# Optimization experiments

Measured on AMD Instinct MI355X. Metric: run time of the kernel, lower is better.

## Reference

```python
import jax, jax.numpy as jnp
import numpy as np


def setup_inputs() -> dict:
    key = jax.random.key(0)
    k1, k2 = jax.random.split(key)
    B, S, D = 4, 8192, 1024
    x = jax.random.normal(k1, (B, S, D), dtype=jnp.float32)
    alpha = jax.random.uniform(k2, (B, S, D), dtype=jnp.float32)
    return {"x": x, "alpha": alpha}


def reference(x, alpha):
    # Linear recurrence h_t = alpha_t * h_{t-1} + x_t, computed as an
    # associative scan over the sequence axis (axis=1).
    def linear_combine(i, j):
        x_i, a_i = i
        x_j, a_j = j
        return (a_j * x_i + x_j, a_j * a_i)

    ys, _ = jax.lax.associative_scan(linear_combine, (x, alpha), axis=1)
    return ys
```

## Files before the change

kernel.cpp:

```cpp
#include <hip/hip_runtime.h>

constexpr int B  = 4;
constexpr int S  = 8192;
constexpr int D  = 1024;
constexpr int C  = 512;
constexpr int L  = S / C;
constexpr int D4 = D / 4;

typedef float nt_float4 __attribute__((ext_vector_type(4)));

__global__ __launch_bounds__(256, 8) void phase1(const float4* __restrict__ x,
                                                 const float4* __restrict__ a,
                                                 float4* __restrict__ Xagg,
                                                 float4* __restrict__ Aagg) {
    const int t = threadIdx.x;
    const int c = blockIdx.x;
    const int b = blockIdx.y;
    const long base = ((long)(b * S + c * L)) * D4 + t;

    float4 X = {0.f, 0.f, 0.f, 0.f};
    float4 A = {1.f, 1.f, 1.f, 1.f};
    #pragma unroll 4
    for (int s = 0; s < L; ++s) {
        float4 xv = x[base + (long)s * D4];
        float4 av = a[base + (long)s * D4];
        X.x = fmaf(av.x, X.x, xv.x);
        X.y = fmaf(av.y, X.y, xv.y);
        X.z = fmaf(av.z, X.z, xv.z);
        X.w = fmaf(av.w, X.w, xv.w);
        A.x *= av.x; A.y *= av.y; A.z *= av.z; A.w *= av.w;
    }
    const long o = ((long)(b * C + c)) * D4 + t;
    Xagg[o] = X;
    Aagg[o] = A;
}

__global__ __launch_bounds__(64) void phase2(float* __restrict__ Xagg,
                                             const float* __restrict__ Aagg) {
    const int g = blockIdx.x * 64 + threadIdx.x;
    const int b = g >> 10;
    const int d = g & (D - 1);
    float*       Xp = Xagg + (long)b * C * D + d;
    const float* Ap = Aagg + (long)b * C * D + d;
    float carry = 0.f;
    for (int c = 0; c < C; c += 4) {
        const long o0 = (long)c * D, o1 = o0 + D, o2 = o1 + D, o3 = o2 + D;
        const float X0 = Xp[o0], X1 = Xp[o1], X2 = Xp[o2], X3 = Xp[o3];
        const float A0 = Ap[o0], A1 = Ap[o1], A2 = Ap[o2], A3 = Ap[o3];
        Xp[o0] = carry; carry = fmaf(A0, carry, X0);
        Xp[o1] = carry; carry = fmaf(A1, carry, X1);
        Xp[o2] = carry; carry = fmaf(A2, carry, X2);
        Xp[o3] = carry; carry = fmaf(A3, carry, X3);
    }
}

__global__ __launch_bounds__(256, 8) void phase3(const float4* __restrict__ x,
                                                 const float4* __restrict__ a,
                                                 const float4* __restrict__ prefix,
                                                 float4* __restrict__ out) {
    const int t = threadIdx.x;
    const int c = blockIdx.x;
    const int b = blockIdx.y;

    float4 h = prefix[((long)(b * C + c)) * D4 + t];
    const long base = ((long)(b * S + c * L)) * D4 + t;
    nt_float4* ntout = (nt_float4*)out;
    #pragma unroll 4
    for (int s = 0; s < L; ++s) {
        float4 xv = x[base + (long)s * D4];
        float4 av = a[base + (long)s * D4];
        h.x = fmaf(av.x, h.x, xv.x);
        h.y = fmaf(av.y, h.y, xv.y);
        h.z = fmaf(av.z, h.z, xv.z);
        h.w = fmaf(av.w, h.w, xv.w);
        nt_float4 hv = {h.x, h.y, h.z, h.w};
        __builtin_nontemporal_store(hv, &ntout[base + (long)s * D4]);
    }
}

extern "C" void kernel_launch(void* const* d_in, const int* in_sizes, int n_in,
                              void* d_out, int out_size, void* d_ws, size_t ws_size,
                              hipStream_t stream) {
    const float4* x = (const float4*)d_in[0];
    const float4* a = (const float4*)d_in[1];
    float4* out = (float4*)d_out;

    float* Xagg = (float*)d_ws;
    float* Aagg = Xagg + (size_t)B * C * D;

    dim3 grid1(C, B);
    phase1<<<grid1, 256, 0, stream>>>(x, a, (float4*)Xagg, (float4*)Aagg);

    phase2<<<(B * D) / 64, 64, 0, stream>>>(Xagg, Aagg);

    phase3<<<grid1, 256, 0, stream>>>(x, a, (const float4*)Xagg, out);
}
```

Baseline: 374.7 us.

## Fuse three-phase scan into single-pass decoupled look-back kernel

Replaces the three kernels (chunk reduce, carry scan, chunk rescan) with a single kernel. It uses a dynamic ticket for block ordering and decoupled look-back through flags that mark whether a chunk's aggregate or its inclusive carry is ready. Each block keeps its 16 timesteps of x and alpha in registers, so the inputs are read from global memory once instead of twice, and two kernel launches go away. In exchange it adds serial dependency chains across blocks with spin-waiting, higher register pressure that lowers occupancy, and a workspace memset on every call.

```diff
diff --git a/kernel.cpp b/kernel.cpp
--- a/kernel.cpp
+++ b/kernel.cpp
@@ -6,74 +6,113 @@
 constexpr int C  = 512;
 constexpr int L  = S / C;
 constexpr int D4 = D / 4;
+constexpr int R  = B * C;
 
 typedef float nt_float4 __attribute__((ext_vector_type(4)));
 
-__global__ __launch_bounds__(256, 8) void phase1(const float4* __restrict__ x,
-                                                 const float4* __restrict__ a,
-                                                 float4* __restrict__ Xagg,
-                                                 float4* __restrict__ Aagg) {
+__device__ __forceinline__ void store2(unsigned long long* p, float a, float b) {
+    union { float f[2]; unsigned long long u; } v; v.f[0] = a; v.f[1] = b;
+    __hip_atomic_store(p, v.u, __ATOMIC_RELAXED, __HIP_MEMORY_SCOPE_AGENT);
+}
+__device__ __forceinline__ void load2(unsigned long long* p, float& a, float& b) {
+    union { float f[2]; unsigned long long u; } v;
+    v.u = __hip_atomic_load(p, __ATOMIC_RELAXED, __HIP_MEMORY_SCOPE_AGENT);
+    a = v.f[0]; b = v.f[1];
+}
+
+__global__ __launch_bounds__(256, 2) void scan_fused(const float4* __restrict__ x,
+                                                     const float4* __restrict__ a,
+                                                     float4* __restrict__ out,
+                                                     unsigned long long* __restrict__ Xagg,
+                                                     unsigned long long* __restrict__ Aagg,
+                                                     unsigned long long* __restrict__ Carr,
+                                                     int* __restrict__ flags,
+                                                     int* __restrict__ ticket) {
     const int t = threadIdx.x;
-    const int c = blockIdx.x;
-    const int b = blockIdx.y;
+    __shared__ int svid;
+    if (t == 0) svid = atomicAdd(ticket, 1);
+    __syncthreads();
+    const int vid = svid;
+    const int b = vid & (B - 1);
+    const int c = vid >> 2;
+    const int r = b * C + c;
+
     const long base = ((long)(b * S + c * L)) * D4 + t;
 
-    float4 X = {0.f, 0.f, 0.f, 0.f};
-    float4 A = {1.f, 1.f, 1.f, 1.f};
-    #pragma unroll 4
+    float4 Xs[L], Ps[L];
+    #pragma unroll
     for (int s = 0; s < L; ++s) {
-        float4 xv = x[base + (long)s * D4];
-        float4 av = a[base + (long)s * D4];
-        X.x = fmaf(av.x, X.x, xv.x);
-        X.y = fmaf(av.y, X.y, xv.y);
-        X.z = fmaf(av.z, X.z, xv.z);
-        X.w = fmaf(av.w, X.w, xv.w);
-        A.x *= av.x; A.y *= av.y; A.z *= av.z; A.w *= av.w;
+        Xs[s] = x[base + (long)s * D4];
+        Ps[s] = a[base + (long)s * D4];
     }
-    const long o = ((long)(b * C + c)) * D4 + t;
-    Xagg[o] = X;
-    Aagg[o] = A;
-}
+    #pragma unroll
+    for (int s = 1; s < L; ++s) {
+        Xs[s].x = fmaf(Ps[s].x, Xs[s-1].x, Xs[s].x);
+        Xs[s].y = fmaf(Ps[s].y, Xs[s-1].y, Xs[s].y);
+        Xs[s].z = fmaf(Ps[s].z, Xs[s-1].z, Xs[s].z);
+        Xs[s].w = fmaf(Ps[s].w, Xs[s-1].w, Xs[s].w);
+        Ps[s].x *= Ps[s-1].x; Ps[s].y *= Ps[s-1].y;
+        Ps[s].z *= Ps[s-1].z; Ps[s].w *= Ps[s-1].w;
+    }
 
-__global__ __launch_bounds__(64) void phase2(float* __restrict__ Xagg,
-                                             const float* __restrict__ Aagg) {
-    const int g = blockIdx.x * 64 + threadIdx.x;
-    const int b = g >> 10;
-    const int d = g & (D - 1);
-    float*       Xp = Xagg + (long)b * C * D + d;
-    const float* Ap = Aagg + (long)b * C * D + d;
-    float carry = 0.f;
-    for (int c = 0; c < C; c += 4) {
-        const long o0 = (long)c * D, o1 = o0 + D, o2 = o1 + D, o3 = o2 + D;
-        const float X0 = Xp[o0], X1 = Xp[o1], X2 = Xp[o2], X3 = Xp[o3];
-        const float A0 = Ap[o0], A1 = Ap[o1], A2 = Ap[o2], A3 = Ap[o3];
-        Xp[o0] = carry; carry = fmaf(A0, carry, X0);
-        Xp[o1] = carry; carry = fmaf(A1, carry, X1);
-        Xp[o2] = carry; carry = fmaf(A2, carry, X2);
-        Xp[o3] = carry; carry = fmaf(A3, carry, X3);
+    if (c > 0) {
+        const long o = ((long)r * D4 + t) * 2;
+        store2(Xagg + o,     Xs[L-1].x, Xs[L-1].y);
+        store2(Xagg + o + 1, Xs[L-1].z, Xs[L-1].w);
+        store2(Aagg + o,     Ps[L-1].x, Ps[L-1].y);
+        store2(Aagg + o + 1, Ps[L-1].z, Ps[L-1].w);
+        __syncthreads();
+        if (t == 0) __hip_atomic_store(&flags[r], 1, __ATOMIC_RELEASE, __HIP_MEMORY_SCOPE_AGENT);
     }
-}
 
-__global__ __launch_bounds__(256, 8) void phase3(const float4* __restrict__ x,
-                                                 const float4* __restrict__ a,
-                                                 const float4* __restrict__ prefix,
-                                                 float4* __restrict__ out) {
-    const int t = threadIdx.x;
-    const int c = blockIdx.x;
-    const int b = blockIdx.y;
+    float4 carry = {0.f, 0.f, 0.f, 0.f};
+    if (c > 0) {
+        float4 Ar = {1.f, 1.f, 1.f, 1.f};
+        float4 Xr = {0.f, 0.f, 0.f, 0.f};
+        for (int k = r - 1;;) {
+            int f;
+            while ((f = __hip_atomic_load(&flags[k], __ATOMIC_RELAXED,
+                                          __HIP_MEMORY_SCOPE_AGENT)) == 0)
+                __builtin_amdgcn_s_sleep(1);
+            const long o = ((long)k * D4 + t) * 2;
+            if (f == 2) {
+                float cx, cy, cz, cw;
+                load2(Carr + o, cx, cy); load2(Carr + o + 1, cz, cw);
+                carry.x = fmaf(Ar.x, cx, Xr.x);
+                carry.y = fmaf(Ar.y, cy, Xr.y);
+                carry.z = fmaf(Ar.z, cz, Xr.z);
+                carry.w = fmaf(Ar.w, cw, Xr.w);
+                break;
+            }
+            float4 Xk, Ak;
+            load2(Xagg + o, Xk.x, Xk.y); load2(Xagg + o + 1, Xk.z, Xk.w);
+            load2(Aagg + o, Ak.x, Ak.y); load2(Aagg + o + 1, Ak.z, Ak.w);
+            Xr.x = fmaf(Ar.x, Xk.x, Xr.x); Xr.y = fmaf(Ar.y, Xk.y, Xr.y);
+            Xr.z = fmaf(Ar.z, Xk.z, Xr.z); Xr.w = fmaf(Ar.w, Xk.w, Xr.w);
+            Ar.x *= Ak.x; Ar.y *= Ak.y; Ar.z *= Ak.z; Ar.w *= Ak.w;
+            --k;
+        }
+    }
 
-    float4 h = prefix[((long)(b * C + c)) * D4 + t];
-    const long base = ((long)(b * S + c * L)) * D4 + t;
+    {
+        const long o = ((long)r * D4 + t) * 2;
+        float4 co;
+        co.x = fmaf(Ps[L-1].x, carry.x, Xs[L-1].x);
+        co.y = fmaf(Ps[L-1].y, carry.y, Xs[L-1].y);
+        co.z = fmaf(Ps[L-1].z, carry.z, Xs[L-1].z);
+        co.w = fmaf(Ps[L-1].w, carry.w, Xs[L-1].w);
+        store2(Carr + o, co.x, co.y); store2(Carr + o + 1, co.z, co.w);
+    }
+    __syncthreads();
+    if (t == 0) __hip_atomic_store(&flags[r], 2, __ATOMIC_RELEASE, __HIP_MEMORY_SCOPE_AGENT);
+
     nt_float4* ntout = (nt_float4*)out;
-    #pragma unroll 4
+    #pragma unroll
     for (int s = 0; s < L; ++s) {
-        float4 xv = x[base + (long)s * D4];
-        float4 av = a[base + (long)s * D4];
-        h.x = fmaf(av.x, h.x, xv.x);
-        h.y = fmaf(av.y, h.y, xv.y);
-        h.z = fmaf(av.z, h.z, xv.z);
-        h.w = fmaf(av.w, h.w, xv.w);
-        nt_float4 hv = {h.x, h.y, h.z, h.w};
+        nt_float4 hv = { fmaf(Ps[s].x, carry.x, Xs[s].x),
+                         fmaf(Ps[s].y, carry.y, Xs[s].y),
+                         fmaf(Ps[s].z, carry.z, Xs[s].z),
+                         fmaf(Ps[s].w, carry.w, Xs[s].w) };
         __builtin_nontemporal_store(hv, &ntout[base + (long)s * D4]);
     }
 }
@@ -85,13 +124,13 @@
     const float4* a = (const float4*)d_in[1];
     float4* out = (float4*)d_out;
 
-    float* Xagg = (float*)d_ws;
-    float* Aagg = Xagg + (size_t)B * C * D;
+    char* ws = (char*)d_ws;
+    int* ticket = (int*)ws;
+    int* flags  = (int*)(ws + 256);
+    unsigned long long* Xagg = (unsigned long long*)(ws + 16384);
+    unsigned long long* Aagg = Xagg + (size_t)R * D4 * 2;
+    unsigned long long* Carr = Aagg + (size_t)R * D4 * 2;
 
-    dim3 grid1(C, B);
-    phase1<<<grid1, 256, 0, stream>>>(x, a, (float4*)Xagg, (float4*)Aagg);
-
-    phase2<<<(B * D) / 64, 64, 0, stream>>>(Xagg, Aagg);
-
-    phase3<<<grid1, 256, 0, stream>>>(x, a, (const float4*)Xagg, out);
+    hipMemsetAsync(ws, 0, 16384, stream);
+    scan_fused<<<dim3(R), 256, 0, stream>>>(x, a, out, Xagg, Aagg, Carr, flags, ticket);
 }
```

New measurement: 550.1 us. +46.8%, slower.

## Fuse three scan phases into one persistent kernel with grid barriers

Applied to the files above, without the earlier changes.

Replaces the three-kernel chunked scan with a single kernel of 256 blocks that syncs through atomic grid barriers. Chunks become longer (128 steps), which shrinks the carry scan across chunks. Loads are issued in double-buffered groups of 8 to keep more memory requests in flight. The change removes launch gaps and the intermediate round trip, but it depends on all 256 blocks being resident at once and adds a memset plus spin barriers. Only 256 blocks of one wave each run, so occupancy drops and memory parallelism may suffer.

```diff
diff --git a/kernel.cpp b/kernel.cpp
--- a/kernel.cpp
+++ b/kernel.cpp
@@ -1,80 +1,145 @@
 #include <hip/hip_runtime.h>
 
-constexpr int B  = 4;
-constexpr int S  = 8192;
-constexpr int D  = 1024;
-constexpr int C  = 512;
-constexpr int L  = S / C;
-constexpr int D4 = D / 4;
+constexpr int B    = 4;
+constexpr int S    = 8192;
+constexpr int D    = 1024;
+constexpr int CB   = 64;
+constexpr int L    = S / CB;
+constexpr int D4   = D / 4;
+constexpr int NBLK = B * CB;
+constexpr int G    = 8;
+constexpr int NG   = L / G;
 
 typedef float nt_float4 __attribute__((ext_vector_type(4)));
 
-__global__ __launch_bounds__(256, 8) void phase1(const float4* __restrict__ x,
-                                                 const float4* __restrict__ a,
-                                                 float4* __restrict__ Xagg,
-                                                 float4* __restrict__ Aagg) {
-    const int t = threadIdx.x;
-    const int c = blockIdx.x;
-    const int b = blockIdx.y;
+__device__ __forceinline__ void ast(float* p, float v) {
+    __hip_atomic_store(p, v, __ATOMIC_RELAXED, __HIP_MEMORY_SCOPE_AGENT);
+}
+__device__ __forceinline__ float ald(const float* p) {
+    return __hip_atomic_load(p, __ATOMIC_RELAXED, __HIP_MEMORY_SCOPE_AGENT);
+}
+
+__device__ __forceinline__ void gridbar(int* bar) {
+    __syncthreads();
+    if (threadIdx.x == 0) {
+        __hip_atomic_fetch_add(bar, 1, __ATOMIC_ACQ_REL, __HIP_MEMORY_SCOPE_AGENT);
+        while (__hip_atomic_load(bar, __ATOMIC_RELAXED, __HIP_MEMORY_SCOPE_AGENT) < NBLK)
+            __builtin_amdgcn_s_sleep(2);
+        __threadfence();
+    }
+    __syncthreads();
+}
+
+__device__ __forceinline__ void issue_grp(const float4* __restrict__ x,
+                                          const float4* __restrict__ a,
+                                          long o, float4 (&bx)[G], float4 (&ba)[G]) {
+    #pragma unroll
+    for (int j = 0; j < G; ++j) {
+        bx[j] = x[o + (long)j * D4];
+        ba[j] = a[o + (long)j * D4];
+    }
+}
+
+__global__ __launch_bounds__(256, 1) void scan_coop(const float4* __restrict__ x,
+                                                    const float4* __restrict__ a,
+                                                    float4* __restrict__ out,
+                                                    float* __restrict__ Xagg,
+                                                    float* __restrict__ Aagg,
+                                                    float* __restrict__ Pref,
+                                                    int* __restrict__ bars) {
+    const int t   = threadIdx.x;
+    const int bid = blockIdx.x;
+    const int b   = bid >> 6;
+    const int c   = bid & (CB - 1);
     const long base = ((long)(b * S + c * L)) * D4 + t;
+
+    float4 bx0[G], ba0[G], bx1[G], ba1[G];
 
     float4 X = {0.f, 0.f, 0.f, 0.f};
     float4 A = {1.f, 1.f, 1.f, 1.f};
-    #pragma unroll 4
-    for (int s = 0; s < L; ++s) {
-        float4 xv = x[base + (long)s * D4];
-        float4 av = a[base + (long)s * D4];
-        X.x = fmaf(av.x, X.x, xv.x);
-        X.y = fmaf(av.y, X.y, xv.y);
-        X.z = fmaf(av.z, X.z, xv.z);
-        X.w = fmaf(av.w, X.w, xv.w);
-        A.x *= av.x; A.y *= av.y; A.z *= av.z; A.w *= av.w;
+    issue_grp(x, a, base, bx0, ba0);
+    #pragma unroll
+    for (int g = 0; g < NG; g += 2) {
+        issue_grp(x, a, base + (long)(g + 1) * G * D4, bx1, ba1);
+        #pragma unroll
+        for (int j = 0; j < G; ++j) {
+            X.x = fmaf(ba0[j].x, X.x, bx0[j].x); A.x *= ba0[j].x;
+            X.y = fmaf(ba0[j].y, X.y, bx0[j].y); A.y *= ba0[j].y;
+            X.z = fmaf(ba0[j].z, X.z, bx0[j].z); A.z *= ba0[j].z;
+            X.w = fmaf(ba0[j].w, X.w, bx0[j].w); A.w *= ba0[j].w;
+        }
+        if (g + 2 < NG) issue_grp(x, a, base + (long)(g + 2) * G * D4, bx0, ba0);
+        #pragma unroll
+        for (int j = 0; j < G; ++j) {
+            X.x = fmaf(ba1[j].x, X.x, bx1[j].x); A.x *= ba1[j].x;
+            X.y = fmaf(ba1[j].y, X.y, bx1[j].y); A.y *= ba1[j].y;
+            X.z = fmaf(ba1[j].z, X.z, bx1[j].z); A.z *= ba1[j].z;
+            X.w = fmaf(ba1[j].w, X.w, bx1[j].w); A.w *= ba1[j].w;
+        }
     }
-    const long o = ((long)(b * C + c)) * D4 + t;
-    Xagg[o] = X;
-    Aagg[o] = A;
-}
+    {
+        float* Xp = Xagg + (long)bid * D + 4 * t;
+        float* Ap = Aagg + (long)bid * D + 4 * t;
+        ast(Xp + 0, X.x); ast(Xp + 1, X.y); ast(Xp + 2, X.z); ast(Xp + 3, X.w);
+        ast(Ap + 0, A.x); ast(Ap + 1, A.y); ast(Ap + 2, A.z); ast(Ap + 3, A.w);
+    }
 
-__global__ __launch_bounds__(64) void phase2(float* __restrict__ Xagg,
-                                             const float* __restrict__ Aagg) {
-    const int g = blockIdx.x * 64 + threadIdx.x;
-    const int b = g >> 10;
-    const int d = g & (D - 1);
-    float*       Xp = Xagg + (long)b * C * D + d;
-    const float* Ap = Aagg + (long)b * C * D + d;
-    float carry = 0.f;
-    for (int c = 0; c < C; c += 4) {
-        const long o0 = (long)c * D, o1 = o0 + D, o2 = o1 + D, o3 = o2 + D;
-        const float X0 = Xp[o0], X1 = Xp[o1], X2 = Xp[o2], X3 = Xp[o3];
-        const float A0 = Ap[o0], A1 = Ap[o1], A2 = Ap[o2], A3 = Ap[o3];
-        Xp[o0] = carry; carry = fmaf(A0, carry, X0);
-        Xp[o1] = carry; carry = fmaf(A1, carry, X1);
-        Xp[o2] = carry; carry = fmaf(A2, carry, X2);
-        Xp[o3] = carry; carry = fmaf(A3, carry, X3);
+    gridbar(bars + 0);
+
+    if (bid < 16) {
+        const int gg = bid * 256 + t;
+        const int sb = gg >> 10;
+        const int d  = gg & (D - 1);
+        const float* Xp = Xagg + (long)sb * CB * D + d;
+        const float* Ap = Aagg + (long)sb * CB * D + d;
+        float*       Pp = Pref + (long)sb * CB * D + d;
+        float carry = 0.f;
+        for (int cc = 0; cc < CB; cc += 8) {
+            float xv[8], av[8];
+            #pragma unroll
+            for (int j = 0; j < 8; ++j) {
+                xv[j] = ald(Xp + (long)(cc + j) * D);
+                av[j] = ald(Ap + (long)(cc + j) * D);
+            }
+            #pragma unroll
+            for (int j = 0; j < 8; ++j) {
+                ast(Pp + (long)(cc + j) * D, carry);
+                carry = fmaf(av[j], carry, xv[j]);
+            }
+        }
     }
-}
 
-__global__ __launch_bounds__(256, 8) void phase3(const float4* __restrict__ x,
-                                                 const float4* __restrict__ a,
-                                                 const float4* __restrict__ prefix,
-                                                 float4* __restrict__ out) {
-    const int t = threadIdx.x;
-    const int c = blockIdx.x;
-    const int b = blockIdx.y;
+    gridbar(bars + 1);
 
-    float4 h = prefix[((long)(b * C + c)) * D4 + t];
-    const long base = ((long)(b * S + c * L)) * D4 + t;
+    float4 h;
+    {
+        const float* Pp = Pref + (long)bid * D + 4 * t;
+        h.x = ald(Pp + 0); h.y = ald(Pp + 1); h.z = ald(Pp + 2); h.w = ald(Pp + 3);
+    }
     nt_float4* ntout = (nt_float4*)out;
-    #pragma unroll 4
-    for (int s = 0; s < L; ++s) {
-        float4 xv = x[base + (long)s * D4];
-        float4 av = a[base + (long)s * D4];
-        h.x = fmaf(av.x, h.x, xv.x);
-        h.y = fmaf(av.y, h.y, xv.y);
-        h.z = fmaf(av.z, h.z, xv.z);
-        h.w = fmaf(av.w, h.w, xv.w);
-        nt_float4 hv = {h.x, h.y, h.z, h.w};
-        __builtin_nontemporal_store(hv, &ntout[base + (long)s * D4]);
+    issue_grp(x, a, base, bx0, ba0);
+    #pragma unroll
+    for (int g = 0; g < NG; g += 2) {
+        issue_grp(x, a, base + (long)(g + 1) * G * D4, bx1, ba1);
+        #pragma unroll
+        for (int j = 0; j < G; ++j) {
+            h.x = fmaf(ba0[j].x, h.x, bx0[j].x);
+            h.y = fmaf(ba0[j].y, h.y, bx0[j].y);
+            h.z = fmaf(ba0[j].z, h.z, bx0[j].z);
+            h.w = fmaf(ba0[j].w, h.w, bx0[j].w);
+            nt_float4 hv = {h.x, h.y, h.z, h.w};
+            __builtin_nontemporal_store(hv, &ntout[base + (long)(g * G + j) * D4]);
+        }
+        if (g + 2 < NG) issue_grp(x, a, base + (long)(g + 2) * G * D4, bx0, ba0);
+        #pragma unroll
+        for (int j = 0; j < G; ++j) {
+            h.x = fmaf(ba1[j].x, h.x, bx1[j].x);
+            h.y = fmaf(ba1[j].y, h.y, bx1[j].y);
+            h.z = fmaf(ba1[j].z, h.z, bx1[j].z);
+            h.w = fmaf(ba1[j].w, h.w, bx1[j].w);
+            nt_float4 hv = {h.x, h.y, h.z, h.w};
+            __builtin_nontemporal_store(hv, &ntout[base + (long)((g + 1) * G + j) * D4]);
+        }
     }
 }
 
@@ -85,13 +150,12 @@
     const float4* a = (const float4*)d_in[1];
     float4* out = (float4*)d_out;
 
-    float* Xagg = (float*)d_ws;
-    float* Aagg = Xagg + (size_t)B * C * D;
+    char* ws = (char*)d_ws;
+    int*   bars = (int*)ws;
+    float* Xagg = (float*)(ws + 4096);
+    float* Aagg = Xagg + (size_t)NBLK * D;
+    float* Pref = Aagg + (size_t)NBLK * D;
 
-    dim3 grid1(C, B);
-    phase1<<<grid1, 256, 0, stream>>>(x, a, (float4*)Xagg, (float4*)Aagg);
-
-    phase2<<<(B * D) / 64, 64, 0, stream>>>(Xagg, Aagg);
-
-    phase3<<<grid1, 256, 0, stream>>>(x, a, (const float4*)Xagg, out);
+    hipMemsetAsync(ws, 0, 4096, stream);
+    scan_coop<<<dim3(NBLK), 256, 0, stream>>>(x, a, out, Xagg, Aagg, Pref, bars);
 }
```

Result: slower. 430.2 us (+14.8%).
